# Kernel optimization log

Measured on AMD Instinct MI355X. Metric: run time of the kernel, lower is better.

## Reference

```python
import jax, jax.numpy as jnp
import numpy as np

N = 1024            # codeword length (power of 2)
NS = 10             # log2(N) butterfly stages
NUM_ITER = 10       # BP iterations
LLR_MAX = 19.3      # internal LLR clipping value
BS = 512            # batch size
FROZEN_POS = np.arange(64)
INFO_POS = np.setdiff1d(np.arange(N), FROZEN_POS)
K = len(INFO_POS)   # 960 information bits

# Precompute the per-stage butterfly gather patterns (static numpy indices).
_ind_range = np.arange(N // 2)
IND_1 = [(_ind_range * 2 - np.mod(_ind_range, 2 ** s)) for s in range(NS)]
IND_2 = [IND_1[s] + 2 ** s for s in range(NS)]
IND_INV = [np.argsort(np.concatenate([IND_1[s], IND_2[s]])) for s in range(NS)]


def _boxplus(x, y):
    # check-node update, matches tf: log(1+exp(x+y)) - log(exp(x)+exp(y))
    x = jnp.clip(x, -LLR_MAX, LLR_MAX)
    y = jnp.clip(y, -LLR_MAX, LLR_MAX)
    return jnp.log(1.0 + jnp.exp(x + y)) - jnp.log(jnp.exp(x) + jnp.exp(y))


def _bp_forward(llr_in):
    llr_ch = -llr_in  # logits -> internal llr sign convention (as in sionna's call)
    bs = llr_ch.shape[0]
    # a-priori right-messages: LLR_MAX at frozen positions, 0 elsewhere
    msg_r_in = jnp.zeros((1, N), jnp.float32).at[:, FROZEN_POS].set(LLR_MAX)
    msg_r_in = jnp.broadcast_to(msg_r_in, (bs, N))

    def one_iter(msg_l_prev, _):
        # msg_l_prev: [NS+1, bs, N]; slot s+1 feeds stage s of the next r-pass.
        # Initialized to zeros, which reproduces the ind_it==0 zero-init branch.
        # ---- right-going (check-node) pass, stages 0..NS-1 ----
        r_msgs = [msg_r_in]  # slot 0
        for s in range(NS):
            l_in = llr_ch if s == NS - 1 else msg_l_prev[s + 1]
            l1, l2 = l_in[:, IND_1[s]], l_in[:, IND_2[s]]
            r_in = r_msgs[s]
            r1, r2 = r_in[:, IND_1[s]], r_in[:, IND_2[s]]
            r1_out = _boxplus(r1, l2 + r2)
            r2_out = _boxplus(r1, l1) + r2
            r_out = jnp.concatenate([r1_out, r2_out], axis=1)[:, IND_INV[s]]
            r_msgs.append(r_out)
        # ---- left-going (bit-node) pass, stages NS-1..0 ----
        l_msgs = [None] * (NS + 1)
        l_msgs[NS] = llr_ch
        for s in range(NS - 1, -1, -1):
            l_in = l_msgs[s + 1]
            l1, l2 = l_in[:, IND_1[s]], l_in[:, IND_2[s]]
            r_in = r_msgs[s]
            r1, r2 = r_in[:, IND_1[s]], r_in[:, IND_2[s]]
            l1_out = _boxplus(l1, l2 + r2)
            l2_out = _boxplus(r1, l1) + l2
            l_msgs[s] = jnp.concatenate([l1_out, l2_out], axis=1)[:, IND_INV[s]]
        return jnp.stack(l_msgs, axis=0), None

    msg_l0 = jnp.zeros((NS + 1, bs, N), jnp.float32)
    msg_l, _ = jax.lax.scan(one_iter, msg_l0, None, length=NUM_ITER)
    u_hat = msg_l[0][:, INFO_POS]  # [bs, k] soft estimates (internal llr domain)
    return -u_hat                   # flip back to input logit convention


def setup_inputs() -> dict:
    key = jax.random.key(0)
    llr_ch = 2.0 * jax.random.normal(key, (BS, N), dtype=jnp.float32)
    return {"llr_ch": llr_ch}


def reference(llr_ch):
    return _bp_forward(llr_ch)
```

## Files before the change

kernel.cpp:

```cpp
#include <hip/hip_runtime.h>

#define BSZ 512
#define KOUT 960
#define EMAX 2.4092698e8f
#define EMIN 4.1506346e-9f

__device__ __forceinline__ float boxpE(float ex, float ey) {
    ex = fminf(fmaxf(ex, EMIN), EMAX);
    ey = fminf(fmaxf(ey, EMIN), EMAX);
    float num = __builtin_fmaf(ex, ey, 1.0f);
    return num * __builtin_amdgcn_rcpf(ex + ey);
}
__device__ __forceinline__ float boxpE_nc(float ex, float ey) {
    float num = __builtin_fmaf(ex, ey, 1.0f);
    return num * __builtin_amdgcn_rcpf(ex + ey);
}

__global__ __launch_bounds__(512, 4) void polar_bp(const float* __restrict__ in,
                                                   float* __restrict__ out) {
    __shared__ float xbA[1024];
    __shared__ float xbB[1024];
    __shared__ float xbC[128];
    __shared__ float sL7[128];
    __shared__ float sL8[256];
    __shared__ float sL9[512];
    __shared__ float sR6[64];

    const int tid = threadIdx.x;
    const float* inb = in + (size_t)blockIdx.x * 1024;
    float llr0 = __expf(-inb[tid]);
    float llr1 = __expf(-inb[512 + tid]);

    float n0 = boxpE(llr0, llr1);
    sL9[tid] = n0;
    xbA[tid] = n0;
    float Li8 = 0.f, Li7 = 0.f, Li6 = 0.f;
    __syncthreads();
    if (tid < 256) {
        Li8 = boxpE_nc(n0, xbA[tid ^ 256]);
        sL8[tid] = Li8;
        xbB[tid] = Li8;
    }
    __syncthreads();
    if (tid < 128) {
        Li7 = boxpE_nc(Li8, xbB[tid ^ 128]);
        sL7[tid] = Li7;
        xbC[tid] = Li7;
    }
    __syncthreads();
    if (tid < 64) Li6 = boxpE_nc(Li7, xbC[tid + 64]);

    float Rs[6];
    if (tid < 64) {
        float Ls[7];
#pragma unroll
        for (int s = 0; s < 7; ++s) Ls[s] = 1.f;
#pragma unroll 1
        for (int it = 0; it < 10; ++it) {
            float r = EMAX;
#pragma unroll
            for (int s = 0; s <= 5; ++s) {
                float lp = __shfl_xor(Ls[s + 1], 1 << s, 64);
                float rp = __shfl_xor(r, 1 << s, 64);
                bool isB = (tid >> s) & 1;
                float x = isB ? rp : r;
                float y = isB ? lp : lp * rp;
                float c = boxpE(x, y);
                r = isB ? c * r : c;
                if (s <= 4) Rs[s + 1] = r;
            }
            if (it == 9) { sR6[tid] = r; break; }
            float Lc = Li6;
#pragma unroll
            for (int s = 5; s >= 1; --s) {
                const int m = 1 << s;
                float rp = __shfl_xor(Rs[s], m, 64);
                float lp = __shfl_xor(Lc, m, 64);
                bool isB = (tid >> s) & 1;
                float x = isB ? rp : Lc;
                float y = isB ? lp : lp * rp;
                float c = boxpE(x, y);
                Lc = isB ? c * Lc : c;
                Ls[s] = Lc;
            }
            Ls[6] = Li6;
        }
    }
    __syncthreads();

    float r6c = sR6[tid & 63];
    float r7c = boxpE(r6c, sL7[(tid & 127) ^ 64]);
    float r8c = boxpE(r7c, sL8[(tid & 255) ^ 128]);
    float r9c = boxpE(r8c, sL9[tid ^ 256]);

    float Lc0 = n0;
    float Lc1 = boxpE(r9c, llr0) * llr1;

    xbA[tid] = Lc0;
    xbA[512 + tid] = Lc1;
    __syncthreads();
    {
        float p0 = xbA[tid ^ 256];
        float p1 = xbA[512 + (tid ^ 256)];
        bool isB = tid >= 256;
        float x0 = isB ? r8c : Lc0;
        float c0 = boxpE(x0, p0);
        Lc0 = isB ? c0 * Lc0 : c0;
        float x1 = isB ? 1.f : Lc1;
        float c1 = boxpE(x1, p1);
        Lc1 = isB ? c1 * Lc1 : c1;
    }

    xbB[tid] = Lc0;
    xbB[512 + tid] = Lc1;
    __syncthreads();
    {
        float p0 = xbB[tid ^ 128];
        float p1 = xbB[512 + (tid ^ 128)];
        bool isB = (tid >> 7) & 1;
        float r1 = (isB && tid < 256) ? r7c : 1.f;
        float x0 = isB ? r1 : Lc0;
        float c0 = boxpE(x0, p0);
        Lc0 = isB ? c0 * Lc0 : c0;
        float x1 = isB ? 1.f : Lc1;
        float c1 = boxpE(x1, p1);
        Lc1 = isB ? c1 * Lc1 : c1;
    }

    xbA[tid] = Lc0;
    xbA[512 + tid] = Lc1;
    __syncthreads();
    {
        float p0 = xbA[tid ^ 64];
        float p1 = xbA[512 + (tid ^ 64)];
        bool isB = (tid >> 6) & 1;
        float r1 = (isB && tid < 128) ? r6c : 1.f;
        float x0 = isB ? r1 : Lc0;
        float c0 = boxpE(x0, p0);
        Lc0 = isB ? c0 * Lc0 : c0;
        float x1 = isB ? 1.f : Lc1;
        float c1 = boxpE(x1, p1);
        Lc1 = isB ? c1 * Lc1 : c1;
    }

#pragma unroll
    for (int s = 5; s >= 1; --s) {
        const int m = 1 << s;
        float rp = 1.f;
        if (tid < 64) rp = __shfl_xor(Rs[s], m, 64);
        float lp0 = __shfl_xor(Lc0, m, 64);
        float lp1 = __shfl_xor(Lc1, m, 64);
        bool isB = (tid >> s) & 1;
        float x0 = isB ? rp : Lc0;
        float y0 = isB ? lp0 : lp0 * rp;
        float c0 = boxpE(x0, y0);
        Lc0 = isB ? c0 * Lc0 : c0;
        float x1 = isB ? 1.f : Lc1;
        float c1 = boxpE(x1, lp1);
        Lc1 = isB ? c1 * Lc1 : c1;
    }

    {
        float lp0 = __shfl_xor(Lc0, 1, 64);
        float lp1 = __shfl_xor(Lc1, 1, 64);
        bool odd = tid & 1;
        float e0 = odd ? Lc0 : boxpE(Lc0, lp0);
        float e1 = odd ? Lc1 : boxpE(Lc1, lp1);
        float o0 = -__logf(e0);
        float o1 = -__logf(e1);
        const size_t ob = (size_t)blockIdx.x * KOUT;
        if (tid >= 64) out[ob + tid - 64] = o0;
        out[ob + 448 + tid] = o1;
    }
}

extern "C" void kernel_launch(void* const* d_in, const int* in_sizes, int n_in,
                              void* d_out, int out_size, void* d_ws, size_t ws_size,
                              hipStream_t stream) {
    const float* in = (const float*)d_in[0];
    float* out = (float*)d_out;
    polar_bp<<<BSZ, 512, 0, stream>>>(in, out);
}
```

Before: 61.25 us.

## Map each codeword to a single wavefront with register-resident butterflies

Each codeword is now handled by one 64-lane wavefront instead of a 512-thread block. Each lane keeps 16 values in registers, so the high butterfly stages become in-register operations and the shared memory buffers and block barriers disappear. Shuffles with xor 1 and 2 are replaced with DPP quad permutes. The trade is less parallelism per codeword (512 single-wave blocks) and more serial work per lane in the outer stages.

```diff
diff --git a/kernel.cpp b/kernel.cpp
--- a/kernel.cpp
+++ b/kernel.cpp
@@ -16,161 +16,134 @@
     return num * __builtin_amdgcn_rcpf(ex + ey);
 }
 
-__global__ __launch_bounds__(512, 4) void polar_bp(const float* __restrict__ in,
-                                                   float* __restrict__ out) {
-    __shared__ float xbA[1024];
-    __shared__ float xbB[1024];
-    __shared__ float xbC[128];
-    __shared__ float sL7[128];
-    __shared__ float sL8[256];
-    __shared__ float sL9[512];
-    __shared__ float sR6[64];
+__device__ __forceinline__ float shx(float v, int m) {
+    if (m == 1)
+        return __int_as_float(__builtin_amdgcn_update_dpp(
+            0, __float_as_int(v), 0xB1 , 0xF, 0xF, true));
+    if (m == 2)
+        return __int_as_float(__builtin_amdgcn_update_dpp(
+            0, __float_as_int(v), 0x4E , 0xF, 0xF, true));
+    return __shfl_xor(v, m, 64);
+}
 
-    const int tid = threadIdx.x;
+__global__ __launch_bounds__(64, 1) void polar_bp(const float* __restrict__ in,
+                                                  float* __restrict__ out) {
+    const int lane = threadIdx.x;
     const float* inb = in + (size_t)blockIdx.x * 1024;
-    float llr0 = __expf(-inb[tid]);
-    float llr1 = __expf(-inb[512 + tid]);
 
-    float n0 = boxpE(llr0, llr1);
-    sL9[tid] = n0;
-    xbA[tid] = n0;
-    float Li8 = 0.f, Li7 = 0.f, Li6 = 0.f;
-    __syncthreads();
-    if (tid < 256) {
-        Li8 = boxpE_nc(n0, xbA[tid ^ 256]);
-        sL8[tid] = Li8;
-        xbB[tid] = Li8;
-    }
-    __syncthreads();
-    if (tid < 128) {
-        Li7 = boxpE_nc(Li8, xbB[tid ^ 128]);
-        sL7[tid] = Li7;
-        xbC[tid] = Li7;
-    }
-    __syncthreads();
-    if (tid < 64) Li6 = boxpE_nc(Li7, xbC[tid + 64]);
+    float e[16];
+#pragma unroll
+    for (int j = 0; j < 16; ++j) e[j] = __expf(-inb[j * 64 + lane]);
 
-    float Rs[6];
-    if (tid < 64) {
-        float Ls[7];
+    float L9[8], L8[4], L7[2];
 #pragma unroll
-        for (int s = 0; s < 7; ++s) Ls[s] = 1.f;
+    for (int j = 0; j < 8; ++j) L9[j] = boxpE(e[j], e[j + 8]);
+#pragma unroll
+    for (int j = 0; j < 4; ++j) L8[j] = boxpE_nc(L9[j], L9[j + 4]);
+#pragma unroll
+    for (int j = 0; j < 2; ++j) L7[j] = boxpE_nc(L8[j], L8[j + 2]);
+    const float Li6 = boxpE_nc(L7[0], L7[1]);
+
+    float Rs[6], r6;
+    float Ls[7];
+#pragma unroll
+    for (int s = 0; s < 7; ++s) Ls[s] = 1.f;
 #pragma unroll 1
-        for (int it = 0; it < 10; ++it) {
-            float r = EMAX;
+    for (int it = 0; it < 10; ++it) {
+        float r = EMAX;
 #pragma unroll
-            for (int s = 0; s <= 5; ++s) {
-                float lp = __shfl_xor(Ls[s + 1], 1 << s, 64);
-                float rp = __shfl_xor(r, 1 << s, 64);
-                bool isB = (tid >> s) & 1;
-                float x = isB ? rp : r;
-                float y = isB ? lp : lp * rp;
-                float c = boxpE(x, y);
-                r = isB ? c * r : c;
-                if (s <= 4) Rs[s + 1] = r;
-            }
-            if (it == 9) { sR6[tid] = r; break; }
-            float Lc = Li6;
+        for (int s = 0; s <= 5; ++s) {
+            float lp = shx(Ls[s + 1], 1 << s);
+            float rp = shx(r, 1 << s);
+            bool isB = (lane >> s) & 1;
+            float x = isB ? rp : r;
+            float y = isB ? lp : lp * rp;
+            float c = boxpE(x, y);
+            r = isB ? c * r : c;
+            if (s <= 4) Rs[s + 1] = r;
+        }
+        if (it == 9) { r6 = r; break; }
+        float Lc = Li6;
 #pragma unroll
-            for (int s = 5; s >= 1; --s) {
-                const int m = 1 << s;
-                float rp = __shfl_xor(Rs[s], m, 64);
-                float lp = __shfl_xor(Lc, m, 64);
-                bool isB = (tid >> s) & 1;
-                float x = isB ? rp : Lc;
-                float y = isB ? lp : lp * rp;
-                float c = boxpE(x, y);
-                Lc = isB ? c * Lc : c;
-                Ls[s] = Lc;
-            }
-            Ls[6] = Li6;
+        for (int s = 5; s >= 1; --s) {
+            const int m = 1 << s;
+            float rp = shx(Rs[s], m);
+            float lp = shx(Lc, m);
+            bool isB = (lane >> s) & 1;
+            float x = isB ? rp : Lc;
+            float y = isB ? lp : lp * rp;
+            float c = boxpE(x, y);
+            Lc = isB ? c * Lc : c;
+            Ls[s] = Lc;
         }
-    }
-    __syncthreads();
-
-    float r6c = sR6[tid & 63];
-    float r7c = boxpE(r6c, sL7[(tid & 127) ^ 64]);
-    float r8c = boxpE(r7c, sL8[(tid & 255) ^ 128]);
-    float r9c = boxpE(r8c, sL9[tid ^ 256]);
-
-    float Lc0 = n0;
-    float Lc1 = boxpE(r9c, llr0) * llr1;
-
-    xbA[tid] = Lc0;
-    xbA[512 + tid] = Lc1;
-    __syncthreads();
-    {
-        float p0 = xbA[tid ^ 256];
-        float p1 = xbA[512 + (tid ^ 256)];
-        bool isB = tid >= 256;
-        float x0 = isB ? r8c : Lc0;
-        float c0 = boxpE(x0, p0);
-        Lc0 = isB ? c0 * Lc0 : c0;
-        float x1 = isB ? 1.f : Lc1;
-        float c1 = boxpE(x1, p1);
-        Lc1 = isB ? c1 * Lc1 : c1;
+        Ls[6] = Li6;
     }
 
-    xbB[tid] = Lc0;
-    xbB[512 + tid] = Lc1;
-    __syncthreads();
-    {
-        float p0 = xbB[tid ^ 128];
-        float p1 = xbB[512 + (tid ^ 128)];
-        bool isB = (tid >> 7) & 1;
-        float r1 = (isB && tid < 256) ? r7c : 1.f;
-        float x0 = isB ? r1 : Lc0;
-        float c0 = boxpE(x0, p0);
-        Lc0 = isB ? c0 * Lc0 : c0;
-        float x1 = isB ? 1.f : Lc1;
-        float c1 = boxpE(x1, p1);
-        Lc1 = isB ? c1 * Lc1 : c1;
+    float r7v[2], r8v[4], r9v[8];
+#pragma unroll
+    for (int t = 0; t < 2; ++t) r7v[t] = boxpE(r6, L7[t ^ 1]);
+#pragma unroll
+    for (int t = 0; t < 4; ++t) r8v[t] = boxpE(r7v[t & 1], L8[t ^ 2]);
+#pragma unroll
+    for (int t = 0; t < 8; ++t) r9v[t] = boxpE(r8v[t & 3], L9[t ^ 4]);
+
+    float Lc[16];
+#pragma unroll
+    for (int j = 0; j < 8; ++j) Lc[j] = L9[j];
+#pragma unroll
+    for (int j = 8; j < 16; ++j) Lc[j] = boxpE(r9v[j - 8], e[j - 8]) * e[j];
+
+    float t8[16];
+#pragma unroll
+    for (int j = 0; j < 16; ++j) {
+        float Lp = Lc[j ^ 4];
+        if (!(j & 4))      t8[j] = boxpE(Lc[j], Lp);
+        else if (j < 8)    t8[j] = boxpE(r8v[j - 4], Lp) * Lc[j];
+        else               t8[j] = Lc[j];
     }
-
-    xbA[tid] = Lc0;
-    xbA[512 + tid] = Lc1;
-    __syncthreads();
-    {
-        float p0 = xbA[tid ^ 64];
-        float p1 = xbA[512 + (tid ^ 64)];
-        bool isB = (tid >> 6) & 1;
-        float r1 = (isB && tid < 128) ? r6c : 1.f;
-        float x0 = isB ? r1 : Lc0;
-        float c0 = boxpE(x0, p0);
-        Lc0 = isB ? c0 * Lc0 : c0;
-        float x1 = isB ? 1.f : Lc1;
-        float c1 = boxpE(x1, p1);
-        Lc1 = isB ? c1 * Lc1 : c1;
+    float t7[16];
+#pragma unroll
+    for (int j = 0; j < 16; ++j) {
+        float Lp = t8[j ^ 2];
+        if (!(j & 2))      t7[j] = boxpE(t8[j], Lp);
+        else if (j < 4)    t7[j] = boxpE(r7v[j - 2], Lp) * t8[j];
+        else               t7[j] = t8[j];
+    }
+#pragma unroll
+    for (int j = 0; j < 16; ++j) {
+        float Lp = t7[j ^ 1];
+        if (!(j & 1))      Lc[j] = boxpE(t7[j], Lp);
+        else if (j == 1)   Lc[j] = boxpE(r6, Lp) * t7[j];
+        else               Lc[j] = t7[j];
     }
 
 #pragma unroll
     for (int s = 5; s >= 1; --s) {
         const int m = 1 << s;
-        float rp = 1.f;
-        if (tid < 64) rp = __shfl_xor(Rs[s], m, 64);
-        float lp0 = __shfl_xor(Lc0, m, 64);
-        float lp1 = __shfl_xor(Lc1, m, 64);
-        bool isB = (tid >> s) & 1;
-        float x0 = isB ? rp : Lc0;
-        float y0 = isB ? lp0 : lp0 * rp;
-        float c0 = boxpE(x0, y0);
-        Lc0 = isB ? c0 * Lc0 : c0;
-        float x1 = isB ? 1.f : Lc1;
-        float c1 = boxpE(x1, lp1);
-        Lc1 = isB ? c1 * Lc1 : c1;
+        float rp = shx(Rs[s], m);
+        bool isB = (lane >> s) & 1;
+        {
+            float lp = shx(Lc[0], m);
+            float x = isB ? rp : Lc[0];
+            float y = isB ? lp : lp * rp;
+            float c = boxpE(x, y);
+            Lc[0] = isB ? c * Lc[0] : c;
+        }
+#pragma unroll
+        for (int j = 1; j < 16; ++j) {
+            float lp = shx(Lc[j], m);
+            float c = boxpE(Lc[j], lp);
+            Lc[j] = isB ? Lc[j] : c;
+        }
     }
 
-    {
-        float lp0 = __shfl_xor(Lc0, 1, 64);
-        float lp1 = __shfl_xor(Lc1, 1, 64);
-        bool odd = tid & 1;
-        float e0 = odd ? Lc0 : boxpE(Lc0, lp0);
-        float e1 = odd ? Lc1 : boxpE(Lc1, lp1);
-        float o0 = -__logf(e0);
-        float o1 = -__logf(e1);
-        const size_t ob = (size_t)blockIdx.x * KOUT;
-        if (tid >= 64) out[ob + tid - 64] = o0;
-        out[ob + 448 + tid] = o1;
+    const size_t ob = (size_t)blockIdx.x * KOUT;
+    const bool odd = lane & 1;
+#pragma unroll
+    for (int j = 1; j < 16; ++j) {
+        float lp = shx(Lc[j], 1);
+        float ev = odd ? Lc[j] : boxpE(Lc[j], lp);
+        out[ob + j * 64 + lane - 64] = -__logf(ev);
     }
 }
 
@@ -179,5 +152,5 @@
                               hipStream_t stream) {
     const float* in = (const float*)d_in[0];
     float* out = (float*)d_out;
-    polar_bp<<<BSZ, 512, 0, stream>>>(in, out);
+    polar_bp<<<BSZ, 64, 0, stream>>>(in, out);
 }
```

Result: no change. 62.26 us (+1.7%).
